# Kernel optimization log

Hardware: AMD Instinct MI355X
Metric: run time of the kernel (lower is better)

The kernel has to match this reference:

```python
import jax, jax.numpy as jnp
import numpy as np

EMBED = 1024
HEADS = 16
HEAD_DIM = EMBED // HEADS


def setup_inputs() -> dict:
    key = jax.random.key(0)
    ks = jax.random.split(key, 9)
    s = 1.0 / np.sqrt(EMBED)
    x = jax.random.normal(ks[0], (2, 2048, EMBED), dtype=jnp.float32)
    Wq = jax.random.uniform(ks[1], (EMBED, EMBED), jnp.float32, -s, s)
    bq = jax.random.uniform(ks[2], (EMBED,), jnp.float32, -s, s)
    Wk = jax.random.uniform(ks[3], (EMBED, EMBED), jnp.float32, -s, s)
    bk = jax.random.uniform(ks[4], (EMBED,), jnp.float32, -s, s)
    Wv = jax.random.uniform(ks[5], (EMBED, EMBED), jnp.float32, -s, s)
    bv = jax.random.uniform(ks[6], (EMBED,), jnp.float32, -s, s)
    Wo = jax.random.uniform(ks[7], (EMBED, EMBED), jnp.float32, -s, s)
    bo = jax.random.uniform(ks[8], (EMBED,), jnp.float32, -s, s)
    return {"x": x, "Wq": Wq, "bq": bq, "Wk": Wk, "bk": bk,
            "Wv": Wv, "bv": bv, "Wo": Wo, "bo": bo}


def reference(x, Wq, bq, Wk, bk, Wv, bv, Wo, bo):
    B, S, E = x.shape
    H, D = HEADS, HEAD_DIM
    # QKV projections, split heads: [B,S,E] -> [B,H,S,D]
    def proj(W, b):
        return (x @ W + b).reshape(B, S, H, D).transpose(0, 2, 1, 3)
    q, k, v = proj(Wq, bq), proj(Wk, bk), proj(Wv, bv)
    scores = jnp.einsum('bhsd,bhtd->bhst', q, k) / jnp.sqrt(jnp.float32(D))
    attn = jax.nn.softmax(scores, axis=-1)
    out = jnp.einsum('bhst,bhtd->bhsd', attn, v)  # [B,H,S,D]
    out = out.transpose(0, 2, 1, 3).reshape(B, S, E)
    return out @ Wo + bo
```

## Files before the change

kernel.cpp:

```cpp
#include <hip/hip_runtime.h>
#include <cstddef>
#include <cstdint>

#define EMB 1024
#define NH 16
#define HD 64
#define SEQ 2048
#define BATCH 2
#define MROWS 4096

typedef unsigned short u16;
typedef __attribute__((ext_vector_type(8))) short short8;
typedef __attribute__((ext_vector_type(4))) short short4v;
typedef __attribute__((ext_vector_type(4))) float floatx4;

#define MFMA32(a,b,c) __builtin_amdgcn_mfma_f32_16x16x32_bf16((a),(b),(c),0,0,0)

#if __has_builtin(__builtin_amdgcn_mfma_f32_16x16x16bf16_1k)
#define PVMFMA(a,b,c) __builtin_amdgcn_mfma_f32_16x16x16bf16_1k((a),(b),(c),0,0,0)
#elif __has_builtin(__builtin_amdgcn_mfma_f32_16x16x16_bf16)
#define PVMFMA(a,b,c) __builtin_amdgcn_mfma_f32_16x16x16_bf16((a),(b),(c),0,0,0)
#else
__device__ __forceinline__ floatx4 pv_mfma_fb(short4v a, short4v b, floatx4 c) {
    short8 a8 = {a.x, a.y, a.z, a.w, 0, 0, 0, 0};
    short8 b8 = {b.x, b.y, b.z, b.w, 0, 0, 0, 0};
    return MFMA32(a8, b8, c);
}
#define PVMFMA(a,b,c) pv_mfma_fb((a),(b),(c))
#endif

__device__ __forceinline__ u16 f2bf(float f) {
    union { float f; uint32_t u; } v; v.f = f;
    return (u16)((v.u + 0x7fffu + ((v.u >> 16) & 1u)) >> 16);
}
__device__ __forceinline__ uint32_t pk_trunc(float a, float b) {
    union { float f; uint32_t u; } va, vb; va.f = a; vb.f = b;
    return __builtin_amdgcn_perm(vb.u, va.u, 0x07060302u);
}
typedef const __attribute__((address_space(1))) void* gptr_t;
typedef __attribute__((address_space(3))) void* lptr_t;
__device__ __forceinline__ void gl2lds16(const void* g, void* l) {
    __builtin_amdgcn_global_load_lds((gptr_t)g, (lptr_t)l, 16, 0, 0);
}

__global__ __launch_bounds__(256) void cvt_x_k(const float* __restrict__ x,
                                               u16* __restrict__ xh) {
    const int stride = gridDim.x * 256 * 8;
    for (int i = (blockIdx.x * 256 + threadIdx.x) * 8; i < MROWS * EMB; i += stride) {
        float4 a = *(const float4*)(x + i);
        float4 b = *(const float4*)(x + i + 4);
        alignas(16) u16 o[8] = {f2bf(a.x), f2bf(a.y), f2bf(a.z), f2bf(a.w),
                                f2bf(b.x), f2bf(b.y), f2bf(b.z), f2bf(b.w)};
        *(uint4*)(xh + i) = *(const uint4*)o;
    }
}

__global__ __launch_bounds__(256) void cvt_wt_k(
    const float* __restrict__ W0, const float* __restrict__ W1,
    const float* __restrict__ W2, const float* __restrict__ W3,
    u16* __restrict__ Wt4) {
    const int z = blockIdx.z;
    const float* W = (z == 0) ? W0 : (z == 1) ? W1 : (z == 2) ? W2 : W3;
    const float scale = (z == 0) ? 0.125f : 1.0f;
    u16* dst = Wt4 + (size_t)z * 1048576;
    __shared__ float Lf[64][65];
    const int kt = blockIdx.y * 64, nt = blockIdx.x * 64;
    const int tid = threadIdx.x;
    {
        const int r = tid >> 2, c4 = (tid & 3) * 16;
        const float* src = W + (size_t)(kt + r) * EMB + nt + c4;
        #pragma unroll
        for (int i = 0; i < 16; i += 4) {
            float4 v = *(const float4*)(src + i);
            Lf[r][c4 + i + 0] = v.x; Lf[r][c4 + i + 1] = v.y;
            Lf[r][c4 + i + 2] = v.z; Lf[r][c4 + i + 3] = v.w;
        }
    }
    __syncthreads();
    const int n = tid >> 2, k4 = (tid & 3) * 16;
    alignas(16) u16 hb[16];
    #pragma unroll
    for (int i = 0; i < 16; ++i) hb[i] = f2bf(Lf[k4 + i][n] * scale);
    const size_t o = (size_t)(nt + n) * EMB + kt + k4;
    *(uint4*)(dst + o) = *(const uint4*)hb;
    *(uint4*)(dst + o + 8) = *(const uint4*)(hb + 8);
}

__global__ __launch_bounds__(256) void gemm_qkv_k(
    const u16* __restrict__ xh, const u16* __restrict__ Wt4,
    const float* __restrict__ b0, const float* __restrict__ b1,
    const float* __restrict__ b2,
    u16* __restrict__ Q, u16* __restrict__ K, u16* __restrict__ V) {
    const int z = blockIdx.z;
    const u16* Wt = Wt4 + (size_t)z * 1048576;
    const float* bias = (z == 0) ? b0 : (z == 1) ? b1 : b2;
    u16* out = (z == 0) ? Q : (z == 1) ? K : V;
    const float bscale = (z == 0) ? 0.125f : 1.0f;
    const int bm = blockIdx.y * 128, bn = blockIdx.x * 128;
    __shared__ alignas(16) u16 As[4096];
    __shared__ alignas(16) u16 Bs[4096];
    const int tid = threadIdx.x;
    const int lane = tid & 63, w = tid >> 6;
    const int l15 = lane & 15, quad = lane >> 4;
    const int wm = (w & 1) * 64, wn = (w >> 1) * 64;

    floatx4 acc[4][4];
    const floatx4 zf = {0.f, 0.f, 0.f, 0.f};
    #pragma unroll
    for (int mt = 0; mt < 4; ++mt)
        #pragma unroll
        for (int nt = 0; nt < 4; ++nt) acc[mt][nt] = zf;

    const int c0 = tid, c1 = tid + 256;
    const int r0 = c0 >> 2, p0 = c0 & 3, cc0 = (p0 - r0 - (r0 >> 2)) & 3;
    const int r1 = c1 >> 2, p1 = c1 & 3, cc1 = (p1 - r1 - (r1 >> 2)) & 3;
    const u16* ag0 = xh + (size_t)(bm + r0) * EMB + cc0 * 8;
    const u16* ag1 = xh + (size_t)(bm + r1) * EMB + cc1 * 8;
    const u16* bg0 = Wt + (size_t)(bn + r0) * EMB + cc0 * 8;
    const u16* bg1 = Wt + (size_t)(bn + r1) * EMB + cc1 * 8;

    for (int kt = 0; kt < EMB; kt += 32) {
        __syncthreads();
        gl2lds16(ag0 + kt, &As[c0 * 8]); gl2lds16(ag1 + kt, &As[c1 * 8]);
        gl2lds16(bg0 + kt, &Bs[c0 * 8]); gl2lds16(bg1 + kt, &Bs[c1 * 8]);
        __syncthreads();
        short8 af[4], bf[4];
        #pragma unroll
        for (int t = 0; t < 4; ++t) {
            const int ra = wm + t * 16 + l15;
            const int rb = wn + t * 16 + l15;
            af[t] = *(const short8*)&As[ra * 32 + ((quad + ra + (ra >> 2)) & 3) * 8];
            bf[t] = *(const short8*)&Bs[rb * 32 + ((quad + rb + (rb >> 2)) & 3) * 8];
        }
        #pragma unroll
        for (int mt = 0; mt < 4; ++mt)
            #pragma unroll
            for (int nt = 0; nt < 4; ++nt)
                acc[mt][nt] = MFMA32(af[mt], bf[nt], acc[mt][nt]);
    }

    #pragma unroll
    for (int nt = 0; nt < 4; ++nt) {
        const int col = bn + wn + nt * 16 + l15;
        const float bv = bias[col] * bscale;
        #pragma unroll
        for (int mt = 0; mt < 4; ++mt) {
            const int row = bm + wm + mt * 16 + quad * 4;
            #pragma unroll
            for (int r = 0; r < 4; ++r)
                out[(size_t)(row + r) * EMB + col] = f2bf(acc[mt][nt][r] + bv);
        }
    }
}

__global__ __launch_bounds__(256) void gemm_o_k(
    const u16* __restrict__ Ag, const u16* __restrict__ Wt,
    const float* __restrict__ bias, float* __restrict__ out) {
    const int bm = blockIdx.y * 128, bn = blockIdx.x * 128;
    __shared__ alignas(16) u16 As[4096];
    __shared__ alignas(16) u16 Bs[4096];
    const int tid = threadIdx.x;
    const int lane = tid & 63, w = tid >> 6;
    const int l15 = lane & 15, quad = lane >> 4;
    const int wm = (w & 1) * 64, wn = (w >> 1) * 64;

    floatx4 acc[4][4];
    const floatx4 zf = {0.f, 0.f, 0.f, 0.f};
    #pragma unroll
    for (int mt = 0; mt < 4; ++mt)
        #pragma unroll
        for (int nt = 0; nt < 4; ++nt) acc[mt][nt] = zf;

    const int c0 = tid, c1 = tid + 256;
    const int r0 = c0 >> 2, p0 = c0 & 3, cc0 = (p0 - r0 - (r0 >> 2)) & 3;
    const int r1 = c1 >> 2, p1 = c1 & 3, cc1 = (p1 - r1 - (r1 >> 2)) & 3;
    const u16* ag0 = Ag + (size_t)(bm + r0) * EMB + cc0 * 8;
    const u16* ag1 = Ag + (size_t)(bm + r1) * EMB + cc1 * 8;
    const u16* bg0 = Wt + (size_t)(bn + r0) * EMB + cc0 * 8;
    const u16* bg1 = Wt + (size_t)(bn + r1) * EMB + cc1 * 8;

    for (int kt = 0; kt < EMB; kt += 32) {
        __syncthreads();
        gl2lds16(ag0 + kt, &As[c0 * 8]); gl2lds16(ag1 + kt, &As[c1 * 8]);
        gl2lds16(bg0 + kt, &Bs[c0 * 8]); gl2lds16(bg1 + kt, &Bs[c1 * 8]);
        __syncthreads();
        short8 af[4], bf[4];
        #pragma unroll
        for (int t = 0; t < 4; ++t) {
            const int ra = wm + t * 16 + l15;
            const int rb = wn + t * 16 + l15;
            af[t] = *(const short8*)&As[ra * 32 + ((quad + ra + (ra >> 2)) & 3) * 8];
            bf[t] = *(const short8*)&Bs[rb * 32 + ((quad + rb + (rb >> 2)) & 3) * 8];
        }
        #pragma unroll
        for (int mt = 0; mt < 4; ++mt)
            #pragma unroll
            for (int nt = 0; nt < 4; ++nt)
                acc[mt][nt] = MFMA32(af[mt], bf[nt], acc[mt][nt]);
    }

    #pragma unroll
    for (int nt = 0; nt < 4; ++nt) {
        const int col = bn + wn + nt * 16 + l15;
        const float bv = bias[col];
        #pragma unroll
        for (int mt = 0; mt < 4; ++mt) {
            const int row = bm + wm + mt * 16 + quad * 4;
            #pragma unroll
            for (int r = 0; r < 4; ++r)
                out[(size_t)(row + r) * EMB + col] = acc[mt][nt][r] + bv;
        }
    }
}

__global__ __launch_bounds__(256) void vtrans_k(const u16* __restrict__ V,
                                                u16* __restrict__ Vt) {
    const int tt = blockIdx.x, h = blockIdx.y, b = blockIdx.z;
    __shared__ u16 Lt[64][72];
    const int tid = threadIdx.x;
    {
        const int r = tid >> 2, c4 = (tid & 3) * 16;
        const u16* src = V + (size_t)(b * SEQ + tt * 64 + r) * EMB + h * HD + c4;
        alignas(16) u16 buf[16];
        *(uint4*)buf = *(const uint4*)src;
        *(uint4*)(buf + 8) = *(const uint4*)(src + 8);
        #pragma unroll
        for (int i = 0; i < 16; ++i) Lt[c4 + i][r] = buf[i];
    }
    __syncthreads();
    const int d = tid >> 2, t4 = (tid & 3) * 16;
    u16* dst = Vt + ((size_t)((b * NH + h) * HD + d)) * SEQ + tt * 64 + t4;
    *(uint4*)dst = *(const uint4*)&Lt[d][t4];
    *(uint4*)(dst + 8) = *(const uint4*)&Lt[d][t4 + 8];
}

__global__ __launch_bounds__(256) void flash_k(
    const u16* __restrict__ Q, const u16* __restrict__ K,
    const u16* __restrict__ Vt, u16* __restrict__ AO) {
    const int qt = blockIdx.x, h = blockIdx.y, b = blockIdx.z;
    __shared__ alignas(16) u16 Ks[4096];
    __shared__ alignas(16) u16 Vs[4096];
    const int tid = threadIdx.x;
    const int lane = tid & 63, w = tid >> 6;
    const int l15 = lane & 15, quad = lane >> 4;

    const u16* qp = Q + (size_t)(b * SEQ + qt * 64 + w * 16 + l15) * EMB + h * HD + quad * 8;
    const short8 qb0 = *(const short8*)qp;
    const short8 qb1 = *(const short8*)(qp + 32);

    const floatx4 zf = {0.f, 0.f, 0.f, 0.f};
    floatx4 oacc[4];
    #pragma unroll
    for (int nt = 0; nt < 4; ++nt) oacc[nt] = zf;
    float l_part = 0.f;

    const int s0 = tid, s1 = tid + 256;
    const int kr0 = s0 >> 3, kc0 = ((s0 & 7) - kr0) & 7;
    const int kr1 = s1 >> 3, kc1 = ((s1 & 7) - kr1) & 7;
    const u16* kg0 = K + (size_t)(b * SEQ + kr0) * EMB + h * HD + kc0 * 8;
    const u16* kg1 = K + (size_t)(b * SEQ + kr1) * EMB + h * HD + kc1 * 8;
    const u16* vg0 = Vt + ((size_t)((b * NH + h) * HD + kr0)) * SEQ + kc0 * 8;
    const u16* vg1 = Vt + ((size_t)((b * NH + h) * HD + kr1)) * SEQ + kc1 * 8;

    for (int kt = 0; kt < SEQ / 64; ++kt) {
        __syncthreads();
        gl2lds16(kg0 + (size_t)kt * 64 * EMB, &Ks[s0 * 8]);
        gl2lds16(kg1 + (size_t)kt * 64 * EMB, &Ks[s1 * 8]);
        gl2lds16(vg0 + kt * 64, &Vs[s0 * 8]);
        gl2lds16(vg1 + kt * 64, &Vs[s1 * 8]);
        __syncthreads();

        floatx4 sa[4];
        #pragma unroll
        for (int mt = 0; mt < 4; ++mt) {
            const int r = mt * 16 + l15;
            const short8 ka0 = *(const short8*)&Ks[r * 64 + ((quad + r) & 7) * 8];
            const short8 ka1 = *(const short8*)&Ks[r * 64 + ((quad + 4 + r) & 7) * 8];
            sa[mt] = MFMA32(ka1, qb1, MFMA32(ka0, qb0, zf));
        }

        short4v pfr[4];
        #pragma unroll
        for (int mt = 0; mt < 4; ++mt) {
            const float e0 = __expf(sa[mt][0]);
            const float e1 = __expf(sa[mt][1]);
            const float e2 = __expf(sa[mt][2]);
            const float e3 = __expf(sa[mt][3]);
            const uint32_t u01 = pk_trunc(e0, e1);
            const uint32_t u23 = pk_trunc(e2, e3);
            union { float f; uint32_t u; } a, bb, c, d;
            a.u = u01 << 16; bb.u = u01 & 0xffff0000u;
            c.u = u23 << 16; d.u = u23 & 0xffff0000u;
            l_part += (a.f + bb.f) + (c.f + d.f);
            union { uint32_t u[2]; short4v s; } pk;
            pk.u[0] = u01; pk.u[1] = u23;
            pfr[mt] = pk.s;
        }

        #pragma unroll
        for (int mt = 0; mt < 4; ++mt) {
            const int c16 = mt * 2 + (quad >> 1);
            const int hof = (quad & 1) * 4;
            #pragma unroll
            for (int nt = 0; nt < 4; ++nt) {
                const int vr = nt * 16 + l15;
                const short4v vb =
                    *(const short4v*)&Vs[vr * 64 + ((c16 + vr) & 7) * 8 + hof];
                oacc[nt] = PVMFMA(pfr[mt], vb, oacc[nt]);
            }
        }
    }

    l_part += __shfl_xor(l_part, 16, 64);
    l_part += __shfl_xor(l_part, 32, 64);

    #pragma unroll
    for (int r = 0; r < 4; ++r) {
        const float lq = __shfl(l_part, quad * 4 + r, 16);
        const float inv = 1.f / lq;
        const size_t o =
            (size_t)(b * SEQ + qt * 64 + w * 16 + quad * 4 + r) * EMB + h * HD + l15;
        #pragma unroll
        for (int nt = 0; nt < 4; ++nt)
            AO[o + nt * 16] = f2bf(oacc[nt][r] * inv);
    }
}

extern "C" void kernel_launch(void* const* d_in, const int* in_sizes, int n_in,
                              void* d_out, int out_size, void* d_ws, size_t ws_size,
                              hipStream_t stream) {
    const float* x  = (const float*)d_in[0];
    const float* Wq = (const float*)d_in[1];
    const float* bq = (const float*)d_in[2];
    const float* Wk = (const float*)d_in[3];
    const float* bk = (const float*)d_in[4];
    const float* Wv = (const float*)d_in[5];
    const float* bv = (const float*)d_in[6];
    const float* Wo = (const float*)d_in[7];
    const float* bo = (const float*)d_in[8];

    u16* ws16 = (u16*)d_ws;
    const size_t P4 = (size_t)MROWS * EMB;
    u16* xh  = ws16;
    u16* Qb  = ws16 + P4;
    u16* Kb  = ws16 + 2 * P4;
    u16* Vb  = ws16 + 3 * P4;
    u16* Vtb = ws16 + 4 * P4;
    u16* Wt4 = ws16 + 5 * P4;

    cvt_x_k<<<1024, 256, 0, stream>>>(x, xh);
    cvt_wt_k<<<dim3(16, 16, 4), 256, 0, stream>>>(Wq, Wk, Wv, Wo, Wt4);
    gemm_qkv_k<<<dim3(8, 32, 3), 256, 0, stream>>>(xh, Wt4, bq, bk, bv, Qb, Kb, Vb);
    vtrans_k<<<dim3(32, 16, 2), 256, 0, stream>>>(Vb, Vtb);
    flash_k<<<dim3(32, 16, 2), 256, 0, stream>>>(Qb, Kb, Vtb, xh);
    gemm_o_k<<<dim3(8, 32, 1), 256, 0, stream>>>(xh, Wt4 + 3 * 1048576, bo, (float*)d_out);
}
```

Before: 214.1 us.

## Fuse V transpose into QKV GEMM, widen K tiles, double flash query rows

The QKV GEMM now loads 64-wide K slices per iteration with an 8-way swizzle and writes V directly in transposed layout, which removes the separate vtrans kernel and its round trip through memory. The flash kernel processes 128 query rows per block (two 16-row groups per wave), so each K/V tile loaded into LDS is reused twice. Softmax now uses exp2f, with log2(e) folded into the Q weight and bias scaling. The output projection uses 128x64 tiles, which doubles the block count. The trade-offs are higher register pressure in flash, uncoalesced 8-byte strided stores for V^T, and larger LDS use per block.

```diff
diff --git a/kernel.cpp b/kernel.cpp
--- a/kernel.cpp
+++ b/kernel.cpp
@@ -8,6 +8,7 @@
 #define SEQ 2048
 #define BATCH 2
 #define MROWS 4096
+#define LOG2E 1.4426950408889634f
 
 typedef unsigned short u16;
 typedef __attribute__((ext_vector_type(8))) short short8;
@@ -61,7 +62,7 @@
     u16* __restrict__ Wt4) {
     const int z = blockIdx.z;
     const float* W = (z == 0) ? W0 : (z == 1) ? W1 : (z == 2) ? W2 : W3;
-    const float scale = (z == 0) ? 0.125f : 1.0f;
+    const float scale = (z == 0) ? 0.125f * LOG2E : 1.0f;
     u16* dst = Wt4 + (size_t)z * 1048576;
     __shared__ float Lf[64][65];
     const int kt = blockIdx.y * 64, nt = blockIdx.x * 64;
@@ -90,148 +91,167 @@
     const u16* __restrict__ xh, const u16* __restrict__ Wt4,
     const float* __restrict__ b0, const float* __restrict__ b1,
     const float* __restrict__ b2,
-    u16* __restrict__ Q, u16* __restrict__ K, u16* __restrict__ V) {
+    u16* __restrict__ Q, u16* __restrict__ K, u16* __restrict__ Vt) {
     const int z = blockIdx.z;
     const u16* Wt = Wt4 + (size_t)z * 1048576;
     const float* bias = (z == 0) ? b0 : (z == 1) ? b1 : b2;
-    u16* out = (z == 0) ? Q : (z == 1) ? K : V;
-    const float bscale = (z == 0) ? 0.125f : 1.0f;
+    const float bscale = (z == 0) ? 0.125f * LOG2E : 1.0f;
     const int bm = blockIdx.y * 128, bn = blockIdx.x * 128;
-    __shared__ alignas(16) u16 As[4096];
+    __shared__ alignas(16) u16 As[8192];
+    __shared__ alignas(16) u16 Bs[8192];
+    const int tid = threadIdx.x;
+    const int lane = tid & 63, w = tid >> 6;
+    const int l15 = lane & 15, quad = lane >> 4;
+    const int wm = (w & 1) * 64, wn = (w >> 1) * 64;
+
+    floatx4 acc[4][4];
+    const floatx4 zf = {0.f, 0.f, 0.f, 0.f};
+    #pragma unroll
+    for (int mt = 0; mt < 4; ++mt)
+        #pragma unroll
+        for (int nt = 0; nt < 4; ++nt) acc[mt][nt] = zf;
+
+    const u16* ag[4]; const u16* bg[4];
+    #pragma unroll
+    for (int j = 0; j < 4; ++j) {
+        const int s = tid + j * 256;
+        const int r = s >> 3, c = ((s & 7) - r) & 7;
+        ag[j] = xh + (size_t)(bm + r) * EMB + c * 8;
+        bg[j] = Wt + (size_t)(bn + r) * EMB + c * 8;
+    }
+
+    for (int kt = 0; kt < EMB; kt += 64) {
+        __syncthreads();
+        #pragma unroll
+        for (int j = 0; j < 4; ++j) {
+            gl2lds16(ag[j] + kt, &As[(tid + j * 256) * 8]);
+            gl2lds16(bg[j] + kt, &Bs[(tid + j * 256) * 8]);
+        }
+        __syncthreads();
+        #pragma unroll
+        for (int ks = 0; ks < 2; ++ks) {
+            short8 af[4], bf[4];
+            #pragma unroll
+            for (int t = 0; t < 4; ++t) {
+                const int ra = wm + t * 16 + l15;
+                const int rb = wn + t * 16 + l15;
+                af[t] = *(const short8*)&As[ra * 64 + ((quad + 4 * ks + ra) & 7) * 8];
+                bf[t] = *(const short8*)&Bs[rb * 64 + ((quad + 4 * ks + rb) & 7) * 8];
+            }
+            #pragma unroll
+            for (int mt = 0; mt < 4; ++mt)
+                #pragma unroll
+                for (int nt = 0; nt < 4; ++nt)
+                    acc[mt][nt] = MFMA32(af[mt], bf[nt], acc[mt][nt]);
+        }
+    }
+
+    if (z != 2) {
+        u16* out = (z == 0) ? Q : K;
+        #pragma unroll
+        for (int nt = 0; nt < 4; ++nt) {
+            const int col = bn + wn + nt * 16 + l15;
+            const float bv = bias[col] * bscale;
+            #pragma unroll
+            for (int mt = 0; mt < 4; ++mt) {
+                const int row = bm + wm + mt * 16 + quad * 4;
+                #pragma unroll
+                for (int r = 0; r < 4; ++r)
+                    out[(size_t)(row + r) * EMB + col] = f2bf(acc[mt][nt][r] + bv);
+            }
+        }
+    } else {
+        #pragma unroll
+        for (int nt = 0; nt < 4; ++nt) {
+            const int col = bn + wn + nt * 16 + l15;
+            const int hh = col >> 6, d = col & 63;
+            const float bv = bias[col];
+            #pragma unroll
+            for (int mt = 0; mt < 4; ++mt) {
+                const int row = bm + wm + mt * 16 + quad * 4;
+                const int bb = row >> 11, t0 = row & 2047;
+                alignas(8) u16 pk4[4];
+                #pragma unroll
+                for (int r = 0; r < 4; ++r) pk4[r] = f2bf(acc[mt][nt][r] + bv);
+                *(uint2*)(Vt + ((size_t)((bb * NH + hh) * HD + d)) * SEQ + t0) =
+                    *(const uint2*)pk4;
+            }
+        }
+    }
+}
+
+__global__ __launch_bounds__(256) void gemm_o_k(
+    const u16* __restrict__ Ag, const u16* __restrict__ Wt,
+    const float* __restrict__ bias, float* __restrict__ out) {
+    const int bm = blockIdx.y * 128, bn = blockIdx.x * 64;
+    __shared__ alignas(16) u16 As[8192];
     __shared__ alignas(16) u16 Bs[4096];
     const int tid = threadIdx.x;
     const int lane = tid & 63, w = tid >> 6;
     const int l15 = lane & 15, quad = lane >> 4;
-    const int wm = (w & 1) * 64, wn = (w >> 1) * 64;
-
-    floatx4 acc[4][4];
+    const int wm = w * 32;
+
+    floatx4 acc[2][4];
     const floatx4 zf = {0.f, 0.f, 0.f, 0.f};
     #pragma unroll
-    for (int mt = 0; mt < 4; ++mt)
+    for (int mt = 0; mt < 2; ++mt)
         #pragma unroll
         for (int nt = 0; nt < 4; ++nt) acc[mt][nt] = zf;
 
-    const int c0 = tid, c1 = tid + 256;
-    const int r0 = c0 >> 2, p0 = c0 & 3, cc0 = (p0 - r0 - (r0 >> 2)) & 3;
-    const int r1 = c1 >> 2, p1 = c1 & 3, cc1 = (p1 - r1 - (r1 >> 2)) & 3;
-    const u16* ag0 = xh + (size_t)(bm + r0) * EMB + cc0 * 8;
-    const u16* ag1 = xh + (size_t)(bm + r1) * EMB + cc1 * 8;
-    const u16* bg0 = Wt + (size_t)(bn + r0) * EMB + cc0 * 8;
-    const u16* bg1 = Wt + (size_t)(bn + r1) * EMB + cc1 * 8;
-
-    for (int kt = 0; kt < EMB; kt += 32) {
-        __syncthreads();
-        gl2lds16(ag0 + kt, &As[c0 * 8]); gl2lds16(ag1 + kt, &As[c1 * 8]);
-        gl2lds16(bg0 + kt, &Bs[c0 * 8]); gl2lds16(bg1 + kt, &Bs[c1 * 8]);
-        __syncthreads();
-        short8 af[4], bf[4];
-        #pragma unroll
-        for (int t = 0; t < 4; ++t) {
-            const int ra = wm + t * 16 + l15;
-            const int rb = wn + t * 16 + l15;
-            af[t] = *(const short8*)&As[ra * 32 + ((quad + ra + (ra >> 2)) & 3) * 8];
-            bf[t] = *(const short8*)&Bs[rb * 32 + ((quad + rb + (rb >> 2)) & 3) * 8];
-        }
-        #pragma unroll
-        for (int mt = 0; mt < 4; ++mt)
-            #pragma unroll
-            for (int nt = 0; nt < 4; ++nt)
-                acc[mt][nt] = MFMA32(af[mt], bf[nt], acc[mt][nt]);
+    const u16* ag[4]; const u16* bg[2];
+    #pragma unroll
+    for (int j = 0; j < 4; ++j) {
+        const int s = tid + j * 256;
+        const int r = s >> 3, c = ((s & 7) - r) & 7;
+        ag[j] = Ag + (size_t)(bm + r) * EMB + c * 8;
+    }
+    #pragma unroll
+    for (int j = 0; j < 2; ++j) {
+        const int s = tid + j * 256;
+        const int r = s >> 3, c = ((s & 7) - r) & 7;
+        bg[j] = Wt + (size_t)(bn + r) * EMB + c * 8;
+    }
+
+    for (int kt = 0; kt < EMB; kt += 64) {
+        __syncthreads();
+        #pragma unroll
+        for (int j = 0; j < 4; ++j) gl2lds16(ag[j] + kt, &As[(tid + j * 256) * 8]);
+        #pragma unroll
+        for (int j = 0; j < 2; ++j) gl2lds16(bg[j] + kt, &Bs[(tid + j * 256) * 8]);
+        __syncthreads();
+        #pragma unroll
+        for (int ks = 0; ks < 2; ++ks) {
+            short8 af[2], bf[4];
+            #pragma unroll
+            for (int t = 0; t < 2; ++t) {
+                const int ra = wm + t * 16 + l15;
+                af[t] = *(const short8*)&As[ra * 64 + ((quad + 4 * ks + ra) & 7) * 8];
+            }
+            #pragma unroll
+            for (int t = 0; t < 4; ++t) {
+                const int rb = t * 16 + l15;
+                bf[t] = *(const short8*)&Bs[rb * 64 + ((quad + 4 * ks + rb) & 7) * 8];
+            }
+            #pragma unroll
+            for (int mt = 0; mt < 2; ++mt)
+                #pragma unroll
+                for (int nt = 0; nt < 4; ++nt)
+                    acc[mt][nt] = MFMA32(af[mt], bf[nt], acc[mt][nt]);
+        }
     }
 
     #pragma unroll
     for (int nt = 0; nt < 4; ++nt) {
-        const int col = bn + wn + nt * 16 + l15;
-        const float bv = bias[col] * bscale;
-        #pragma unroll
-        for (int mt = 0; mt < 4; ++mt) {
-            const int row = bm + wm + mt * 16 + quad * 4;
-            #pragma unroll
-            for (int r = 0; r < 4; ++r)
-                out[(size_t)(row + r) * EMB + col] = f2bf(acc[mt][nt][r] + bv);
-        }
-    }
-}
-
-__global__ __launch_bounds__(256) void gemm_o_k(
-    const u16* __restrict__ Ag, const u16* __restrict__ Wt,
-    const float* __restrict__ bias, float* __restrict__ out) {
-    const int bm = blockIdx.y * 128, bn = blockIdx.x * 128;
-    __shared__ alignas(16) u16 As[4096];
-    __shared__ alignas(16) u16 Bs[4096];
-    const int tid = threadIdx.x;
-    const int lane = tid & 63, w = tid >> 6;
-    const int l15 = lane & 15, quad = lane >> 4;
-    const int wm = (w & 1) * 64, wn = (w >> 1) * 64;
-
-    floatx4 acc[4][4];
-    const floatx4 zf = {0.f, 0.f, 0.f, 0.f};
-    #pragma unroll
-    for (int mt = 0; mt < 4; ++mt)
-        #pragma unroll
-        for (int nt = 0; nt < 4; ++nt) acc[mt][nt] = zf;
-
-    const int c0 = tid, c1 = tid + 256;
-    const int r0 = c0 >> 2, p0 = c0 & 3, cc0 = (p0 - r0 - (r0 >> 2)) & 3;
-    const int r1 = c1 >> 2, p1 = c1 & 3, cc1 = (p1 - r1 - (r1 >> 2)) & 3;
-    const u16* ag0 = Ag + (size_t)(bm + r0) * EMB + cc0 * 8;
-    const u16* ag1 = Ag + (size_t)(bm + r1) * EMB + cc1 * 8;
-    const u16* bg0 = Wt + (size_t)(bn + r0) * EMB + cc0 * 8;
-    const u16* bg1 = Wt + (size_t)(bn + r1) * EMB + cc1 * 8;
-
-    for (int kt = 0; kt < EMB; kt += 32) {
-        __syncthreads();
-        gl2lds16(ag0 + kt, &As[c0 * 8]); gl2lds16(ag1 + kt, &As[c1 * 8]);
-        gl2lds16(bg0 + kt, &Bs[c0 * 8]); gl2lds16(bg1 + kt, &Bs[c1 * 8]);
-        __syncthreads();
-        short8 af[4], bf[4];
-        #pragma unroll
-        for (int t = 0; t < 4; ++t) {
-            const int ra = wm + t * 16 + l15;
-            const int rb = wn + t * 16 + l15;
-            af[t] = *(const short8*)&As[ra * 32 + ((quad + ra + (ra >> 2)) & 3) * 8];
-            bf[t] = *(const short8*)&Bs[rb * 32 + ((quad + rb + (rb >> 2)) & 3) * 8];
-        }
-        #pragma unroll
-        for (int mt = 0; mt < 4; ++mt)
-            #pragma unroll
-            for (int nt = 0; nt < 4; ++nt)
-                acc[mt][nt] = MFMA32(af[mt], bf[nt], acc[mt][nt]);
-    }
-
-    #pragma unroll
-    for (int nt = 0; nt < 4; ++nt) {
-        const int col = bn + wn + nt * 16 + l15;
+        const int col = bn + nt * 16 + l15;
         const float bv = bias[col];
         #pragma unroll
-        for (int mt = 0; mt < 4; ++mt) {
+        for (int mt = 0; mt < 2; ++mt) {
             const int row = bm + wm + mt * 16 + quad * 4;
             #pragma unroll
             for (int r = 0; r < 4; ++r)
                 out[(size_t)(row + r) * EMB + col] = acc[mt][nt][r] + bv;
         }
     }
-}
-
-__global__ __launch_bounds__(256) void vtrans_k(const u16* __restrict__ V,
-                                                u16* __restrict__ Vt) {
-    const int tt = blockIdx.x, h = blockIdx.y, b = blockIdx.z;
-    __shared__ u16 Lt[64][72];
-    const int tid = threadIdx.x;
-    {
-        const int r = tid >> 2, c4 = (tid & 3) * 16;
-        const u16* src = V + (size_t)(b * SEQ + tt * 64 + r) * EMB + h * HD + c4;
-        alignas(16) u16 buf[16];
-        *(uint4*)buf = *(const uint4*)src;
-        *(uint4*)(buf + 8) = *(const uint4*)(src + 8);
-        #pragma unroll
-        for (int i = 0; i < 16; ++i) Lt[c4 + i][r] = buf[i];
-    }
-    __syncthreads();
-    const int d = tid >> 2, t4 = (tid & 3) * 16;
-    u16* dst = Vt + ((size_t)((b * NH + h) * HD + d)) * SEQ + tt * 64 + t4;
-    *(uint4*)dst = *(const uint4*)&Lt[d][t4];
-    *(uint4*)(dst + 8) = *(const uint4*)&Lt[d][t4 + 8];
 }
 
 __global__ __launch_bounds__(256) void flash_k(
@@ -244,15 +264,20 @@
     const int lane = tid & 63, w = tid >> 6;
     const int l15 = lane & 15, quad = lane >> 4;
 
-    const u16* qp = Q + (size_t)(b * SEQ + qt * 64 + w * 16 + l15) * EMB + h * HD + quad * 8;
-    const short8 qb0 = *(const short8*)qp;
-    const short8 qb1 = *(const short8*)(qp + 32);
+    const u16* qp = Q + (size_t)(b * SEQ + qt * 128 + w * 32 + l15) * EMB + h * HD + quad * 8;
+    short8 qb[2][2];
+    qb[0][0] = *(const short8*)qp;
+    qb[0][1] = *(const short8*)(qp + 32);
+    qb[1][0] = *(const short8*)(qp + 16 * EMB);
+    qb[1][1] = *(const short8*)(qp + 16 * EMB + 32);
 
     const floatx4 zf = {0.f, 0.f, 0.f, 0.f};
-    floatx4 oacc[4];
-    #pragma unroll
-    for (int nt = 0; nt < 4; ++nt) oacc[nt] = zf;
-    float l_part = 0.f;
+    floatx4 oacc[2][4];
+    float l_part[2] = {0.f, 0.f};
+    #pragma unroll
+    for (int u = 0; u < 2; ++u)
+        #pragma unroll
+        for (int nt = 0; nt < 4; ++nt) oacc[u][nt] = zf;
 
     const int s0 = tid, s1 = tid + 256;
     const int kr0 = s0 >> 3, kc0 = ((s0 & 7) - kr0) & 7;
@@ -270,32 +295,36 @@
         gl2lds16(vg1 + kt * 64, &Vs[s1 * 8]);
         __syncthreads();
 
-        floatx4 sa[4];
+        floatx4 sa[2][4];
         #pragma unroll
         for (int mt = 0; mt < 4; ++mt) {
             const int r = mt * 16 + l15;
             const short8 ka0 = *(const short8*)&Ks[r * 64 + ((quad + r) & 7) * 8];
             const short8 ka1 = *(const short8*)&Ks[r * 64 + ((quad + 4 + r) & 7) * 8];
-            sa[mt] = MFMA32(ka1, qb1, MFMA32(ka0, qb0, zf));
-        }
-
-        short4v pfr[4];
-        #pragma unroll
-        for (int mt = 0; mt < 4; ++mt) {
-            const float e0 = __expf(sa[mt][0]);
-            const float e1 = __expf(sa[mt][1]);
-            const float e2 = __expf(sa[mt][2]);
-            const float e3 = __expf(sa[mt][3]);
-            const uint32_t u01 = pk_trunc(e0, e1);
-            const uint32_t u23 = pk_trunc(e2, e3);
-            union { float f; uint32_t u; } a, bb, c, d;
-            a.u = u01 << 16; bb.u = u01 & 0xffff0000u;
-            c.u = u23 << 16; d.u = u23 & 0xffff0000u;
-            l_part += (a.f + bb.f) + (c.f + d.f);
-            union { uint32_t u[2]; short4v s; } pk;
-            pk.u[0] = u01; pk.u[1] = u23;
-            pfr[mt] = pk.s;
-        }
+            #pragma unroll
+            for (int u = 0; u < 2; ++u)
+                sa[u][mt] = MFMA32(ka1, qb[u][1], MFMA32(ka0, qb[u][0], zf));
+        }
+
+        short4v pfr[2][4];
+        #pragma unroll
+        for (int u = 0; u < 2; ++u)
+            #pragma unroll
+            for (int mt = 0; mt < 4; ++mt) {
+                const float e0 = exp2f(sa[u][mt][0]);
+                const float e1 = exp2f(sa[u][mt][1]);
+                const float e2 = exp2f(sa[u][mt][2]);
+                const float e3 = exp2f(sa[u][mt][3]);
+                const uint32_t u01 = pk_trunc(e0, e1);
+                const uint32_t u23 = pk_trunc(e2, e3);
+                union { float f; uint32_t u; } a, bb, c, d;
+                a.u = u01 << 16; bb.u = u01 & 0xffff0000u;
+                c.u = u23 << 16; d.u = u23 & 0xffff0000u;
+                l_part[u] += (a.f + bb.f) + (c.f + d.f);
+                union { uint32_t uu[2]; short4v s; } pk;
+                pk.uu[0] = u01; pk.uu[1] = u23;
+                pfr[u][mt] = pk.s;
+            }
 
         #pragma unroll
         for (int mt = 0; mt < 4; ++mt) {
@@ -306,24 +335,31 @@
                 const int vr = nt * 16 + l15;
                 const short4v vb =
                     *(const short4v*)&Vs[vr * 64 + ((c16 + vr) & 7) * 8 + hof];
-                oacc[nt] = PVMFMA(pfr[mt], vb, oacc[nt]);
-            }
-        }
-    }
-
-    l_part += __shfl_xor(l_part, 16, 64);
-    l_part += __shfl_xor(l_part, 32, 64);
-
-    #pragma unroll
-    for (int r = 0; r < 4; ++r) {
-        const float lq = __shfl(l_part, quad * 4 + r, 16);
-        const float inv = 1.f / lq;
-        const size_t o =
-            (size_t)(b * SEQ + qt * 64 + w * 16 + quad * 4 + r) * EMB + h * HD + l15;
-        #pragma unroll
-        for (int nt = 0; nt < 4; ++nt)
-            AO[o + nt * 16] = f2bf(oacc[nt][r] * inv);
-    }
+                #pragma unroll
+                for (int u = 0; u < 2; ++u)
+                    oacc[u][nt] = PVMFMA(pfr[u][mt], vb, oacc[u][nt]);
+            }
+        }
+    }
+
+    #pragma unroll
+    for (int u = 0; u < 2; ++u) {
+        l_part[u] += __shfl_xor(l_part[u], 16, 64);
+        l_part[u] += __shfl_xor(l_part[u], 32, 64);
+    }
+
+    #pragma unroll
+    for (int u = 0; u < 2; ++u)
+        #pragma unroll
+        for (int r = 0; r < 4; ++r) {
+            const float lq = __shfl(l_part[u], quad * 4 + r, 16);
+            const float inv = 1.f / lq;
+            const size_t o = (size_t)(b * SEQ + qt * 128 + w * 32 + u * 16 + quad * 4 + r) * EMB
+                           + h * HD + l15;
+            #pragma unroll
+            for (int nt = 0; nt < 4; ++nt)
+                AO[o + nt * 16] = f2bf(oacc[u][nt][r] * inv);
+        }
 }
 
 extern "C" void kernel_launch(void* const* d_in, const int* in_sizes, int n_in,
@@ -344,14 +380,12 @@
     u16* xh  = ws16;
     u16* Qb  = ws16 + P4;
     u16* Kb  = ws16 + 2 * P4;
-    u16* Vb  = ws16 + 3 * P4;
-    u16* Vtb = ws16 + 4 * P4;
-    u16* Wt4 = ws16 + 5 * P4;
+    u16* Vtb = ws16 + 3 * P4;
+    u16* Wt4 = ws16 + 4 * P4;
 
     cvt_x_k<<<1024, 256, 0, stream>>>(x, xh);
     cvt_wt_k<<<dim3(16, 16, 4), 256, 0, stream>>>(Wq, Wk, Wv, Wo, Wt4);
-    gemm_qkv_k<<<dim3(8, 32, 3), 256, 0, stream>>>(xh, Wt4, bq, bk, bv, Qb, Kb, Vb);
-    vtrans_k<<<dim3(32, 16, 2), 256, 0, stream>>>(Vb, Vtb);
-    flash_k<<<dim3(32, 16, 2), 256, 0, stream>>>(Qb, Kb, Vtb, xh);
-    gemm_o_k<<<dim3(8, 32, 1), 256, 0, stream>>>(xh, Wt4 + 3 * 1048576, bo, (float*)d_out);
-}
+    gemm_qkv_k<<<dim3(8, 32, 3), 256, 0, stream>>>(xh, Wt4, bq, bk, bv, Qb, Kb, Vtb);
+    flash_k<<<dim3(16, 16, 2), 256, 0, stream>>>(Qb, Kb, Vtb, xh);
+    gemm_o_k<<<dim3(16, 32, 1), 256, 0, stream>>>(xh, Wt4 + 3 * 1048576, bo, (float*)d_out);
+}
```

New measurement: 237.7 us. 1.11x slower.
